# Optimization experiments

Measured on AMD Instinct MI355X. Metric: run time of the kernel, lower is better.

## Reference

```python
import jax, jax.numpy as jnp
import numpy as np

N_EDGE_TYPES = 25
EF = 2  # edge feature dim (excluding type)
HID = 10


def _edge_nn(et, ef, emb, wh, bh, wg, bg):
    # y = relu(emb[et] * (ef@Wh+bh) + (ef@Wg+bg)) -> [E, in*out]
    return jax.nn.relu(emb[et] * (ef @ wh + bh) + (ef @ wg + bg))


def _nnconv(x, et, ef, src, dst, emb, wh, bh, wg, bg, root, bias, in_c, out_c):
    n = x.shape[0]
    w = _edge_nn(et, ef, emb, wh, bh, wg, bg).reshape(-1, in_c, out_c)  # [E,in,out]
    msg = jnp.einsum('ei,eio->eo', x[src], w)                          # per-edge matmul
    s = jax.ops.segment_sum(msg, dst, num_segments=n)
    cnt = jax.ops.segment_sum(jnp.ones((src.shape[0],), x.dtype), dst, num_segments=n)
    agg = s / jnp.maximum(cnt, 1.0)[:, None]                           # scatter-mean
    return agg + x @ root + bias


def _make_params(key, in_c, out_c):
    ks = jax.random.split(key, 6)
    d = in_c * out_c
    s = 0.1
    return dict(
        emb=jax.random.normal(ks[0], (N_EDGE_TYPES, d), jnp.float32) * s,
        wh=jax.random.normal(ks[1], (EF, d), jnp.float32) * s,
        bh=jax.random.normal(ks[2], (d,), jnp.float32) * s,
        wg=jax.random.normal(ks[3], (EF, d), jnp.float32) * s,
        bg=jax.random.normal(ks[4], (d,), jnp.float32) * s,
        root=jax.random.normal(ks[5], (in_c, out_c), jnp.float32) * s,
        bias=jnp.zeros((out_c,), jnp.float32),
    )


def setup_inputs() -> dict:
    key = jax.random.key(0)
    ks = jax.random.split(key, 12)
    N, E, IN_C, OUT_C, B = 50000, 250000, 16, 16, 8
    inp = {
        'x': jax.random.normal(ks[0], (N, IN_C), jnp.float32),
        'edge_feat': jax.random.normal(ks[1], (E, EF), jnp.float32),
        'edge_type': jax.random.randint(ks[2], (E,), 0, N_EDGE_TYPES),
        'edge_src': jax.random.randint(ks[3], (E,), 0, N),
        'edge_dst': jax.random.randint(ks[4], (E,), 0, N),
        'cell_type': jax.random.randint(ks[5], (N,), 0, 3),
        'batch_ids': jnp.sort(jax.random.randint(ks[6], (N,), 0, B)),
        'batch_size': B,
    }
    for i, (ic, oc) in enumerate([(IN_C, HID), (HID, HID), (HID, OUT_C)], start=1):
        p = _make_params(ks[6 + i], ic, oc)
        for k, v in p.items():
            inp[f'{k}{i}'] = v
    return inp


def reference(x, edge_feat,
              emb1, wh1, bh1, wg1, bg1, root1, bias1,
              emb2, wh2, bh2, wg2, bg2, root2, bias2,
              emb3, wh3, bh3, wg3, bg3, root3, bias3,
              edge_type, edge_src, edge_dst, cell_type, batch_ids, batch_size):
    in_c, out_c = x.shape[1], root3.shape[1]
    h = _nnconv(x, edge_type, edge_feat, edge_src, edge_dst,
                emb1, wh1, bh1, wg1, bg1, root1, bias1, in_c, HID)
    h = jax.nn.relu(h)  # dropout is identity in eval mode
    h = _nnconv(h, edge_type, edge_feat, edge_src, edge_dst,
                emb2, wh2, bh2, wg2, bg2, root2, bias2, HID, HID)
    h = jax.nn.relu(h)
    h = _nnconv(h, edge_type, edge_feat, edge_src, edge_dst,
                emb3, wh3, bh3, wg3, bg3, root3, bias3, HID, out_c)
    h = jax.nn.relu(h)
    # scatter-mean pooling over nodes with cell_type==1, grouped by graph id
    gate = (cell_type == 1).astype(jnp.int32)
    idx = gate * (batch_ids.astype(jnp.int32) + 1)  # 0 = discarded bucket
    nseg = batch_size + 1
    s = jax.ops.segment_sum(h, idx, num_segments=nseg)
    cnt = jax.ops.segment_sum(jnp.ones((h.shape[0],), h.dtype), idx, num_segments=nseg)
    pooled = s / jnp.maximum(cnt, 1.0)[:, None]
    return pooled[1:batch_size + 1, :]  # [B, out_c]
```

## Files before the change

kernel.cpp:

```cpp
#include <hip/hip_runtime.h>

#define IN1 16
#define HIDC 10
#define OUT3 16
#define NTYPES 25
#define MAXB 32
#define HSTR 12

__global__ __launch_bounds__(256) void hist_kernel(const int* __restrict__ edst,
                                                   int* __restrict__ deg,
                                                   int* __restrict__ pos, int E) {
  int e = blockIdx.x * blockDim.x + threadIdx.x;
  if (e < E) pos[e] = atomicAdd(&deg[edst[e]], 1);
}

__global__ __launch_bounds__(1024) void scan_kernel(const int4* __restrict__ deg4,
                                                    int* __restrict__ row_ptr, int N) {
  __shared__ int wsums[16];
  __shared__ int s_run;
  int tid = threadIdx.x, lane = tid & 63, wid = tid >> 6;
  if (tid == 0) s_run = 0;
  __syncthreads();
  int N4 = (N + 3) >> 2;
  for (int base = 0; base < N4; base += 1024) {
    int i4 = base + tid;
    int4 v = make_int4(0, 0, 0, 0);
    if (i4 < N4) v = deg4[i4];
    int idx0 = i4 * 4;
    if (idx0 + 1 >= N) v.y = 0;
    if (idx0 + 2 >= N) v.z = 0;
    if (idx0 + 3 >= N) v.w = 0;
    int s = v.x + v.y + v.z + v.w;
    int x = s;
    #pragma unroll
    for (int off = 1; off < 64; off <<= 1) {
      int y = __shfl_up(x, off);
      if (lane >= off) x += y;
    }
    if (lane == 63) wsums[wid] = x;
    __syncthreads();
    if (tid < 16) {
      int w = wsums[tid];
      #pragma unroll
      for (int off = 1; off < 16; off <<= 1) {
        int y = __shfl_up(w, off);
        if (tid >= off) w += y;
      }
      wsums[tid] = w;
    }
    __syncthreads();
    int excl = x - s + ((wid > 0) ? wsums[wid - 1] : 0) + s_run;
    int total = wsums[15];
    if (idx0 < N) row_ptr[idx0] = excl;
    if (idx0 + 1 < N) row_ptr[idx0 + 1] = excl + v.x;
    if (idx0 + 2 < N) row_ptr[idx0 + 2] = excl + v.x + v.y;
    if (idx0 + 3 < N) row_ptr[idx0 + 3] = excl + v.x + v.y + v.z;
    __syncthreads();
    if (tid == 0) s_run += total;
    __syncthreads();
  }
  if (threadIdx.x == 0) row_ptr[N] = s_run;
}

__global__ __launch_bounds__(256) void permute_kernel(
    const int* __restrict__ edst, const int* __restrict__ esrc,
    const int* __restrict__ et, const float2* __restrict__ ef,
    const int* __restrict__ row_ptr, const int* __restrict__ pos,
    int4* __restrict__ edges, int E) {
  int e = blockIdx.x * blockDim.x + threadIdx.x;
  if (e >= E) return;
  int d = edst[e];
  int idx = row_ptr[d] + pos[e];
  float2 f = ef[e];
  int4 r;
  r.x = esrc[e];
  r.y = et[e];
  r.z = __float_as_int(f.x);
  r.w = __float_as_int(f.y);
  edges[idx] = r;
}

template<int IN_C, int O>
__device__ void pack_one(int t, const float* emb, const float* wh, const float* bh,
                         const float* wg, const float* bg,
                         float4* gAB, float2* gC) {
  constexpr int D = IN_C * O;
  constexpr int NI2 = IN_C / 2;
  for (int idx = threadIdx.x; idx < NI2 * O; idx += 256) {
    int i2 = idx / O, o = idx - i2 * O;
    int k0 = (2 * i2) * O + o, k1 = k0 + O;
    float e0 = emb[t * D + k0], e1 = emb[t * D + k1];
    float a0 = fmaf(e0, wh[k0], wg[k0]);
    float b0 = fmaf(e0, wh[D + k0], wg[D + k0]);
    float c0 = fmaf(e0, bh[k0], bg[k0]);
    float a1 = fmaf(e1, wh[k1], wg[k1]);
    float b1 = fmaf(e1, wh[D + k1], wg[D + k1]);
    float c1 = fmaf(e1, bh[k1], bg[k1]);
    int kk = (i2 * NTYPES + t) * O + o;
    gAB[kk] = make_float4(a0, b0, a1, b1);
    gC[kk] = make_float2(c0, c1);
  }
}

__global__ __launch_bounds__(256) void pack_zero_kernel(
    const float* __restrict__ emb1, const float* __restrict__ wh1,
    const float* __restrict__ bh1, const float* __restrict__ wg1, const float* __restrict__ bg1,
    const float* __restrict__ emb2, const float* __restrict__ wh2,
    const float* __restrict__ bh2, const float* __restrict__ wg2, const float* __restrict__ bg2,
    const float* __restrict__ emb3, const float* __restrict__ wh3,
    const float* __restrict__ bh3, const float* __restrict__ wg3, const float* __restrict__ bg3,
    float4* __restrict__ gAB1, float2* __restrict__ gC1,
    float4* __restrict__ gAB2, float2* __restrict__ gC2,
    float4* __restrict__ gAB3, float2* __restrict__ gC3,
    int* __restrict__ za, int na, int* __restrict__ zb, int nb)
{
  if (blockIdx.x < NTYPES) {
    int t = blockIdx.x;
    pack_one<IN1, HIDC>(t, emb1, wh1, bh1, wg1, bg1, gAB1, gC1);
    pack_one<HIDC, HIDC>(t, emb2, wh2, bh2, wg2, bg2, gAB2, gC2);
    pack_one<HIDC, OUT3>(t, emb3, wh3, bh3, wg3, bg3, gAB3, gC3);
  } else {
    int bi = blockIdx.x - NTYPES;
    int nthr = (gridDim.x - NTYPES) * 256;
    for (int i = bi * 256 + threadIdx.x; i < na; i += nthr) za[i] = 0;
    for (int i = bi * 256 + threadIdx.x; i < nb; i += nthr) zb[i] = 0;
  }
}

template<int IN_C, int XSTR, int O, int IPG, int NPW, bool POOL>
__global__ __launch_bounds__(512, 6) void layer_kernel(
    const float* __restrict__ xin,
    const int4* __restrict__ edges,
    const int* __restrict__ row_ptr,
    const float4* __restrict__ gAB,
    const float2* __restrict__ gC,
    const float* __restrict__ root,
    const float* __restrict__ bias,
    float* __restrict__ hout,
    const int* __restrict__ ctype, const int* __restrict__ bids,
    float* __restrict__ pcnt, int N, int B)
{
  constexpr int NI2 = IN_C / 2;
  constexpr int SZ = NI2 * NTYPES * O;
  constexpr int JMAX = (IPG == 4) ? 2 : 3;
  constexpr int NPB = 8 * NPW;
  __shared__ __align__(16) float4 s_AB[SZ];
  __shared__ __align__(16) float2 s_C[SZ];
  __shared__ float s_root[IN_C * O];
  __shared__ float s_bias[O];
  __shared__ float s_psum[POOL ? (MAXB * 16) : 1];
  __shared__ float s_pcnt[POOL ? MAXB : 1];

  int tid = threadIdx.x;
  for (int k = tid; k < SZ; k += 512) s_AB[k] = gAB[k];
  {
    const float4* gc4 = (const float4*)gC;
    float4* sc4 = (float4*)s_C;
    for (int k = tid; k < SZ / 2; k += 512) sc4[k] = gc4[k];
  }
  for (int k = tid; k < IN_C * O; k += 512) s_root[k] = root[k];
  if (tid < O) s_bias[tid] = bias[tid];
  if (POOL) {
    for (int i = tid; i < MAXB * 16; i += 512) s_psum[i] = 0.f;
    for (int i = tid; i < MAXB; i += 512) s_pcnt[i] = 0.f;
  }
  __syncthreads();

  int wave = tid >> 6, lane = tid & 63;
  int slot = lane / (16 * IPG);
  int rem = lane % (16 * IPG);
  int ig = rem >> 4;
  int o = rem & 15;
  int oc = (o < O) ? o : (O - 1);

  int npair, i2b, ch0;
  if (IPG == 4) { npair = 2; i2b = ig * 2; ch0 = ig * 4; }
  else { npair = (ig == 0) ? 3 : 2; i2b = (ig == 0) ? 0 : 3; ch0 = (ig == 0) ? 0 : 6; }

  int n = blockIdx.x * NPB + wave * NPW + slot;
  int start = 0, end = 0;
  if (n < N) { start = row_ptr[n]; end = row_ptr[n + 1]; }

  auto body = [&](int4 cur, float& a) {
    int src = cur.x, t = cur.y;
    float f0 = __int_as_float(cur.z), f1 = __int_as_float(cur.w);
    const float* __restrict__ xr = xin + (size_t)src * XSTR + ch0;
    float xv[2 * JMAX];
    if (IPG == 4) {
      float4 v = *(const float4*)xr;
      xv[0] = v.x; xv[1] = v.y; xv[2] = v.z; xv[3] = v.w;
    } else {
      const float2* x2 = (const float2*)xr;
      float2 p0 = x2[0], p1 = x2[1], p2 = x2[2];
      xv[0] = p0.x; xv[1] = p0.y; xv[2] = p1.x; xv[3] = p1.y; xv[4] = p2.x; xv[5] = p2.y;
    }
    int kb = t * O + oc;
    #pragma unroll
    for (int j = 0; j < JMAX; ++j) {
      bool on = (IPG == 4) || (j < npair);
      if (on) {
        int k = (i2b + j) * (NTYPES * O) + kb;
        float4 ab = s_AB[k];
        float2 c2 = s_C[k];
        float w0 = fmaxf(fmaf(f0, ab.x, fmaf(f1, ab.y, c2.x)), 0.f);
        float w1 = fmaxf(fmaf(f0, ab.z, fmaf(f1, ab.w, c2.y)), 0.f);
        a = fmaf(xv[2 * j], w0, a);
        a = fmaf(xv[2 * j + 1], w1, a);
      }
    }
  };

  float acc0 = 0.f, acc1 = 0.f;
  int e = start;
  for (; e + 1 < end; e += 2) {
    int4 c0 = edges[e];
    int4 c1 = edges[e + 1];
    body(c0, acc0);
    body(c1, acc1);
  }
  if (e < end) body(edges[e], acc0);
  float acc = acc0 + acc1;

  acc += __shfl_xor(acc, 16);
  if (IPG == 4) acc += __shfl_xor(acc, 32);

  if (n < N && ig == 0 && o < O) {
    float inv = 1.0f / fmaxf((float)(end - start), 1.0f);
    float v = fmaf(acc, inv, s_bias[o]);
    const float* __restrict__ xr = xin + (size_t)n * XSTR;
    #pragma unroll
    for (int i = 0; i < IN_C; ++i) v = fmaf(xr[i], s_root[i * O + o], v);
    v = fmaxf(v, 0.f);
    if (!POOL) {
      hout[(size_t)n * HSTR + o] = v;
    } else if (ctype[n] == 1) {
      int b = bids[n];
      atomicAdd(&s_psum[b * 16 + o], v);
      if (o == 0) atomicAdd(&s_pcnt[b], 1.0f);
    }
  }

  if (POOL) {
    __syncthreads();
    for (int i = tid; i < B * 16; i += 512) {
      float v = s_psum[i];
      if (v != 0.f) atomicAdd(&hout[i], v);
    }
    for (int i = tid; i < B; i += 512) {
      float c = s_pcnt[i];
      if (c != 0.f) atomicAdd(&pcnt[i], c);
    }
  }
}

__global__ __launch_bounds__(256) void finalize_kernel(
    const float* __restrict__ psum, const float* __restrict__ pcnt,
    float* __restrict__ out, int B) {
  int i = blockIdx.x * blockDim.x + threadIdx.x;
  if (i >= B * OUT3) return;
  int b = i / OUT3;
  out[i] = psum[i] / fmaxf(pcnt[b], 1.0f);
}

extern "C" void kernel_launch(void* const* d_in, const int* in_sizes, int n_in,
                              void* d_out, int out_size, void* d_ws, size_t ws_size,
                              hipStream_t stream)
{
  const float* x     = (const float*)d_in[0];
  const float* ef    = (const float*)d_in[1];
  const int*   et    = (const int*)d_in[2];
  const int*   esrc  = (const int*)d_in[3];
  const int*   edst  = (const int*)d_in[4];
  const int*   ctype = (const int*)d_in[5];
  const int*   bids  = (const int*)d_in[6];
  const float* emb1 = (const float*)d_in[8];
  const float* wh1  = (const float*)d_in[9];
  const float* bh1  = (const float*)d_in[10];
  const float* wg1  = (const float*)d_in[11];
  const float* bg1  = (const float*)d_in[12];
  const float* root1= (const float*)d_in[13];
  const float* bias1= (const float*)d_in[14];
  const float* emb2 = (const float*)d_in[15];
  const float* wh2  = (const float*)d_in[16];
  const float* bh2  = (const float*)d_in[17];
  const float* wg2  = (const float*)d_in[18];
  const float* bg2  = (const float*)d_in[19];
  const float* root2= (const float*)d_in[20];
  const float* bias2= (const float*)d_in[21];
  const float* emb3 = (const float*)d_in[22];
  const float* wh3  = (const float*)d_in[23];
  const float* bh3  = (const float*)d_in[24];
  const float* wg3  = (const float*)d_in[25];
  const float* bg3  = (const float*)d_in[26];
  const float* root3= (const float*)d_in[27];
  const float* bias3= (const float*)d_in[28];

  const int N = in_sizes[0] / IN1;
  const int E = in_sizes[2];
  const int B = out_size / OUT3;

  int4* edges   = (int4*)d_ws;
  int*  deg     = (int*)(edges + E);
  int*  pos     = deg + N;
  int*  row_ptr = pos + E;
  int   np1r    = ((N + 1 + 3) / 4) * 4;
  float* h1     = (float*)(row_ptr + np1r);
  float* h2     = h1 + (size_t)N * HSTR;
  float* psum   = h2 + (size_t)N * HSTR;
  float* pcnt   = psum + (size_t)B * 16;
  float* pk     = pcnt + B;
  float4* gAB1 = (float4*)pk;
  float2* gC1  = (float2*)(pk + 8000);
  float4* gAB2 = (float4*)(pk + 12000);
  float2* gC2  = (float2*)(pk + 17000);
  float4* gAB3 = (float4*)(pk + 19504);
  float2* gC3  = (float2*)(pk + 27504);

  pack_zero_kernel<<<160, 256, 0, stream>>>(
      emb1, wh1, bh1, wg1, bg1, emb2, wh2, bh2, wg2, bg2, emb3, wh3, bh3, wg3, bg3,
      gAB1, gC1, gAB2, gC2, gAB3, gC3,
      deg, N, (int*)psum, B * 16 + B);
  hist_kernel<<<(E + 255) / 256, 256, 0, stream>>>(edst, deg, pos, E);
  scan_kernel<<<1, 1024, 0, stream>>>((const int4*)deg, row_ptr, N);
  permute_kernel<<<(E + 255) / 256, 256, 0, stream>>>(
      edst, esrc, et, (const float2*)ef, row_ptr, pos, edges, E);

  layer_kernel<IN1, 16, HIDC, 4, 1, false><<<(N + 7) / 8, 512, 0, stream>>>(
      x, edges, row_ptr, gAB1, gC1, root1, bias1, h1, nullptr, nullptr, nullptr, N, B);
  layer_kernel<HIDC, HSTR, HIDC, 2, 2, false><<<(N + 15) / 16, 512, 0, stream>>>(
      h1, edges, row_ptr, gAB2, gC2, root2, bias2, h2, nullptr, nullptr, nullptr, N, B);
  layer_kernel<HIDC, HSTR, OUT3, 2, 2, true><<<(N + 15) / 16, 512, 0, stream>>>(
      h2, edges, row_ptr, gAB3, gC3, root3, bias3, psum, ctype, bids, pcnt, N, B);

  finalize_kernel<<<1, 256, 0, stream>>>(psum, pcnt, (float*)d_out, B);
}
```

Measured before the change: 302.4 us.

## Read packed edge weights from global cache and fold finalize into last block

Removes the per-block shared-memory staging of the packed edge-network tables, root and bias. Edge-weight lookups now go straight to global memory and rely on the L1/L2 caches, which cuts the startup load and barrier in every block and lets more blocks stay resident (launch bounds go from 6 to 8). The separate finalize kernel is replaced by a last-block-done counter in the pooling layer, saving one launch. The cost is per-edge gathers from global memory instead of LDS, and fences plus atomics in the pooling layer.

```diff
diff --git a/kernel.cpp b/kernel.cpp
--- a/kernel.cpp
+++ b/kernel.cpp
@@ -128,7 +128,7 @@
 }
 
 template<int IN_C, int XSTR, int O, int IPG, int NPW, bool POOL>
-__global__ __launch_bounds__(512, 6) void layer_kernel(
+__global__ __launch_bounds__(512, 8) void layer_kernel(
     const float* __restrict__ xin,
     const int4* __restrict__ edges,
     const int* __restrict__ row_ptr,
@@ -138,33 +138,22 @@
     const float* __restrict__ bias,
     float* __restrict__ hout,
     const int* __restrict__ ctype, const int* __restrict__ bids,
-    float* __restrict__ pcnt, int N, int B)
+    float* __restrict__ pcnt,
+    int* __restrict__ done,
+    float* __restrict__ out,
+    int N, int B)
 {
-  constexpr int NI2 = IN_C / 2;
-  constexpr int SZ = NI2 * NTYPES * O;
   constexpr int JMAX = (IPG == 4) ? 2 : 3;
   constexpr int NPB = 8 * NPW;
-  __shared__ __align__(16) float4 s_AB[SZ];
-  __shared__ __align__(16) float2 s_C[SZ];
-  __shared__ float s_root[IN_C * O];
-  __shared__ float s_bias[O];
   __shared__ float s_psum[POOL ? (MAXB * 16) : 1];
   __shared__ float s_pcnt[POOL ? MAXB : 1];
 
   int tid = threadIdx.x;
-  for (int k = tid; k < SZ; k += 512) s_AB[k] = gAB[k];
-  {
-    const float4* gc4 = (const float4*)gC;
-    float4* sc4 = (float4*)s_C;
-    for (int k = tid; k < SZ / 2; k += 512) sc4[k] = gc4[k];
-  }
-  for (int k = tid; k < IN_C * O; k += 512) s_root[k] = root[k];
-  if (tid < O) s_bias[tid] = bias[tid];
   if (POOL) {
     for (int i = tid; i < MAXB * 16; i += 512) s_psum[i] = 0.f;
     for (int i = tid; i < MAXB; i += 512) s_pcnt[i] = 0.f;
-  }
-  __syncthreads();
+    __syncthreads();
+  }
 
   int wave = tid >> 6, lane = tid & 63;
   int slot = lane / (16 * IPG);
@@ -200,8 +189,8 @@
       bool on = (IPG == 4) || (j < npair);
       if (on) {
         int k = (i2b + j) * (NTYPES * O) + kb;
-        float4 ab = s_AB[k];
-        float2 c2 = s_C[k];
+        float4 ab = gAB[k];
+        float2 c2 = gC[k];
         float w0 = fmaxf(fmaf(f0, ab.x, fmaf(f1, ab.y, c2.x)), 0.f);
         float w1 = fmaxf(fmaf(f0, ab.z, fmaf(f1, ab.w, c2.y)), 0.f);
         a = fmaf(xv[2 * j], w0, a);
@@ -226,10 +215,10 @@
 
   if (n < N && ig == 0 && o < O) {
     float inv = 1.0f / fmaxf((float)(end - start), 1.0f);
-    float v = fmaf(acc, inv, s_bias[o]);
+    float v = fmaf(acc, inv, bias[o]);
     const float* __restrict__ xr = xin + (size_t)n * XSTR;
     #pragma unroll
-    for (int i = 0; i < IN_C; ++i) v = fmaf(xr[i], s_root[i * O + o], v);
+    for (int i = 0; i < IN_C; ++i) v = fmaf(xr[i], root[i * O + o], v);
     v = fmaxf(v, 0.f);
     if (!POOL) {
       hout[(size_t)n * HSTR + o] = v;
@@ -250,16 +239,16 @@
       float c = s_pcnt[i];
       if (c != 0.f) atomicAdd(&pcnt[i], c);
     }
-  }
-}
-
-__global__ __launch_bounds__(256) void finalize_kernel(
-    const float* __restrict__ psum, const float* __restrict__ pcnt,
-    float* __restrict__ out, int B) {
-  int i = blockIdx.x * blockDim.x + threadIdx.x;
-  if (i >= B * OUT3) return;
-  int b = i / OUT3;
-  out[i] = psum[i] / fmaxf(pcnt[b], 1.0f);
+    __threadfence();
+    __shared__ int s_last;
+    if (tid == 0) s_last = (atomicAdd(done, 1) == (int)gridDim.x - 1);
+    __syncthreads();
+    if (s_last && tid < B * 16) {
+      float v = atomicAdd(&hout[tid], 0.f);
+      float c = atomicAdd(&pcnt[tid >> 4], 0.f);
+      out[tid] = v / fmaxf(c, 1.0f);
+    }
+  }
 }
 
 extern "C" void kernel_launch(void* const* d_in, const int* in_sizes, int n_in,
@@ -308,7 +297,8 @@
   float* h2     = h1 + (size_t)N * HSTR;
   float* psum   = h2 + (size_t)N * HSTR;
   float* pcnt   = psum + (size_t)B * 16;
-  float* pk     = pcnt + B;
+  int*   done   = (int*)(pcnt + B);
+  float* pk     = (float*)(done + 4);
   float4* gAB1 = (float4*)pk;
   float2* gC1  = (float2*)(pk + 8000);
   float4* gAB2 = (float4*)(pk + 12000);
@@ -319,18 +309,19 @@
   pack_zero_kernel<<<160, 256, 0, stream>>>(
       emb1, wh1, bh1, wg1, bg1, emb2, wh2, bh2, wg2, bg2, emb3, wh3, bh3, wg3, bg3,
       gAB1, gC1, gAB2, gC2, gAB3, gC3,
-      deg, N, (int*)psum, B * 16 + B);
+      deg, N, (int*)psum, B * 16 + B + 4);
   hist_kernel<<<(E + 255) / 256, 256, 0, stream>>>(edst, deg, pos, E);
   scan_kernel<<<1, 1024, 0, stream>>>((const int4*)deg, row_ptr, N);
   permute_kernel<<<(E + 255) / 256, 256, 0, stream>>>(
       edst, esrc, et, (const float2*)ef, row_ptr, pos, edges, E);
 
   layer_kernel<IN1, 16, HIDC, 4, 1, false><<<(N + 7) / 8, 512, 0, stream>>>(
-      x, edges, row_ptr, gAB1, gC1, root1, bias1, h1, nullptr, nullptr, nullptr, N, B);
+      x, edges, row_ptr, gAB1, gC1, root1, bias1, h1,
+      nullptr, nullptr, nullptr, nullptr, nullptr, N, B);
   layer_kernel<HIDC, HSTR, HIDC, 2, 2, false><<<(N + 15) / 16, 512, 0, stream>>>(
-      h1, edges, row_ptr, gAB2, gC2, root2, bias2, h2, nullptr, nullptr, nullptr, N, B);
+      h1, edges, row_ptr, gAB2, gC2, root2, bias2, h2,
+      nullptr, nullptr, nullptr, nullptr, nullptr, N, B);
   layer_kernel<HIDC, HSTR, OUT3, 2, 2, true><<<(N + 15) / 16, 512, 0, stream>>>(
-      h2, edges, row_ptr, gAB3, gC3, root3, bias3, psum, ctype, bids, pcnt, N, B);
-
-  finalize_kernel<<<1, 256, 0, stream>>>(psum, pcnt, (float*)d_out, B);
-}
+      h2, edges, row_ptr, gAB3, gC3, root3, bias3, psum,
+      ctype, bids, pcnt, done, (float*)d_out, N, B);
+}
```

Measured after the change: 724.1 us. 139% more time.
